# Kernel optimization log

Measured on AMD Instinct MI355X. Metric: run time of the kernel, lower is better.

Reference implementation:

```python
import jax, jax.numpy as jnp
import numpy as np
from jax import lax

H = 1024
L = 9


def setup_inputs() -> dict:
    key = jax.random.key(0)
    ks = jax.random.split(key, 10)
    B, T = 64, 512
    hidden_states = jax.random.normal(ks[0], (B, T, H), dtype=jnp.float32)
    attention_mask = jnp.ones((B, T), dtype=jnp.int32)
    labels = jax.random.randint(ks[1], (B, T), 0, L).astype(jnp.int64)
    W1 = 0.02 * jax.random.normal(ks[2], (H, H // 2), dtype=jnp.float32)
    b1 = jnp.zeros((H // 2,), dtype=jnp.float32)
    W2 = 0.02 * jax.random.normal(ks[3], (H // 2, L), dtype=jnp.float32)
    b2 = jnp.zeros((L,), dtype=jnp.float32)
    start_transitions = 0.1 * jax.random.normal(ks[4], (L,), dtype=jnp.float32)
    end_transitions = 0.1 * jax.random.normal(ks[5], (L,), dtype=jnp.float32)
    transitions = 0.1 * jax.random.normal(ks[6], (L, L), dtype=jnp.float32)
    return {"hidden_states": hidden_states, "attention_mask": attention_mask,
            "labels": labels, "W1": W1, "b1": b1, "W2": W2, "b2": b2,
            "start_transitions": start_transitions,
            "end_transitions": end_transitions, "transitions": transitions}


def crf_nll(logits, tags, mask, start_t, end_t, trans):
    """torchcrf negative mean log-likelihood. logits [B,T,L], tags [B,T], mask [B,T] bool."""
    emis = jnp.swapaxes(logits, 0, 1)          # [T,B,L]
    tg = jnp.swapaxes(tags, 0, 1)              # [T,B]
    m = jnp.swapaxes(mask, 0, 1).astype(logits.dtype)  # [T,B]

    # --- numerator: score of the gold path ---
    e0 = jnp.take_along_axis(emis[0], tg[0][:, None], axis=1)[:, 0]
    score0 = start_t[tg[0]] + e0

    def num_step(carry, inp):
        score, prev = carry
        e, t, mi = inp
        step = trans[prev, t] + jnp.take_along_axis(e, t[:, None], axis=1)[:, 0]
        score = score + step * mi
        prev = jnp.where(mi > 0, t, prev)
        return (score, prev), None

    (num, last_tag), _ = lax.scan(num_step, (score0, tg[0]), (emis[1:], tg[1:], m[1:]))
    num = num + end_t[last_tag]

    # --- denominator: forward algorithm (log partition) ---
    alpha0 = start_t[None, :] + emis[0]        # [B,L]

    def den_step(alpha, inp):
        e, mi = inp
        nxt = jax.nn.logsumexp(alpha[:, :, None] + trans[None, :, :] + e[:, None, :], axis=1)
        return jnp.where(mi[:, None] > 0, nxt, alpha), None

    alpha, _ = lax.scan(den_step, alpha0, (emis[1:], m[1:]))
    den = jax.nn.logsumexp(alpha + end_t[None, :], axis=1)

    return -jnp.mean(num - den)


def reference(hidden_states, attention_mask, labels, W1, b1, W2, b2,
              start_transitions, end_transitions, transitions):
    # dropout is identity in eval mode
    x = jax.nn.relu(hidden_states @ W1 + b1)
    logits = x @ W2 + b2                        # [B,T,L]

    valid = labels != -100
    crf_labels = jnp.where(valid, labels, 0)
    mask = (attention_mask.astype(bool)) & valid
    mask = mask.at[:, 0].set(True)              # first timestep always on

    loss = crf_nll(logits, crf_labels, mask,
                   start_transitions, end_transitions, transitions)
    return logits, loss
```

## Files before the change

### kernel.cpp

```cpp
#include <hip/hip_runtime.h>

#define T_  512
#define H_  1024
#define HC  512

typedef short short8 __attribute__((ext_vector_type(8)));
typedef float f32x16 __attribute__((ext_vector_type(16)));

__device__ __forceinline__ unsigned short f2bf(float x) {
  unsigned u = __float_as_uint(x);
  u += 0x7FFFu + ((u >> 16) & 1u);
  return (unsigned short)(u >> 16);
}
__device__ __forceinline__ float bf2f(unsigned short h) {
  return __uint_as_float(((unsigned)h) << 16);
}
__device__ __forceinline__ unsigned cvtpk(float lo, float hi) {
  unsigned r;
  asm("v_cvt_pk_bf16_f32 %0, %1, %2" : "=v"(r) : "v"(lo), "v"(hi));
  return r;
}
__device__ __forceinline__ void gload_lds16(const void* g, void* l) {
  __builtin_amdgcn_global_load_lds((const __attribute__((address_space(1))) unsigned*)g,
                                   (__attribute__((address_space(3))) unsigned*)l, 16, 0, 0);
}

__global__ void conv_w1(const float* __restrict__ w1, unsigned short* __restrict__ w1b) {
  int idx = blockIdx.x * 256 + threadIdx.x;
  int n = idx & 511, o = idx >> 9;
  const float* src = w1 + (size_t)(o * 8) * HC + n;
  float v[8];
  #pragma unroll
  for (int j = 0; j < 8; ++j) v[j] = src[j * HC];
  uint4 d;
  d.x = cvtpk(v[0], v[1]);
  d.y = cvtpk(v[2], v[3]);
  d.z = cvtpk(v[4], v[5]);
  d.w = cvtpk(v[6], v[7]);
  *(uint4*)(w1b + (size_t)idx * 8) = d;
}

__global__ __launch_bounds__(256, 2) void gemm1(
    const float* __restrict__ hs, const unsigned short* __restrict__ w1b,
    const float* __restrict__ b1, const float* __restrict__ w2,
    const float* __restrict__ b2, float* __restrict__ logits, float* __restrict__ wsE)
{
  __shared__ __align__(16) unsigned char smem[80128];
  const int tid  = threadIdx.x;
  const int lane = tid & 63;
  const int w    = tid >> 6;
  const int row0 = blockIdx.x * 64;

  f32x16 acc[2][4];
  #pragma unroll
  for (int m = 0; m < 2; ++m)
    #pragma unroll
    for (int n = 0; n < 4; ++n)
      #pragma unroll
      for (int e = 0; e < 16; ++e) acc[m][n][e] = 0.f;

  const int ar  = tid >> 2;
  const int akg = tid & 3;
  const float* aSrc = hs + (size_t)(row0 + ar) * H_ + akg * 8;
  const int aoff = ar * 64 + ((akg ^ ((ar >> 1) & 3)) * 16);

  {
    float4 av0 = *(const float4*)(aSrc);
    float4 av1 = *(const float4*)(aSrc + 4);
    unsigned char* bbase = smem + 4096;
    #pragma unroll
    for (int i = 0; i < 8; ++i) {
      int kg = i >> 1;
      int c0 = ((i & 1) * 4 + w) * 64;
      gload_lds16(w1b + ((size_t)kg * 512 + c0 + lane) * 8, bbase + (kg * 512 + c0) * 16);
    }
    uint4 ap;
    ap.x = cvtpk(av0.x, av0.y); ap.y = cvtpk(av0.z, av0.w);
    ap.z = cvtpk(av1.x, av1.y); ap.w = cvtpk(av1.z, av1.w);
    *(uint4*)(smem + aoff) = ap;
  }

  for (int kt = 0; kt < 31; ++kt) {
    const int cur = kt & 1, nxt = cur ^ 1;
    float4 av0 = *(const float4*)(aSrc + (kt + 1) * 32);
    float4 av1 = *(const float4*)(aSrc + (kt + 1) * 32 + 4);
    {
      unsigned char* bbase = smem + nxt * 36864 + 4096;
      int o0 = (kt + 1) * 4;
      #pragma unroll
      for (int i = 0; i < 8; ++i) {
        int kg = i >> 1;
        int c0 = ((i & 1) * 4 + w) * 64;
        gload_lds16(w1b + ((size_t)(o0 + kg) * 512 + c0 + lane) * 8,
                    bbase + (kg * 512 + c0) * 16);
      }
    }
    asm volatile("s_waitcnt vmcnt(10) lgkmcnt(0)" ::: "memory");
    __builtin_amdgcn_s_barrier();
    __builtin_amdgcn_sched_barrier(0);
    {
      const unsigned char* abase = smem + cur * 36864;
      const unsigned char* bbase = abase + 4096;
      #pragma unroll
      for (int ks = 0; ks < 2; ++ks) {
        const int kg = ks * 2 + (lane >> 5);
        short8 aF[2], bF[4];
        #pragma unroll
        for (int m = 0; m < 2; ++m) {
          int r = m * 32 + (lane & 31);
          aF[m] = *(const short8*)(abase + r * 64 + ((kg ^ ((r >> 1) & 3)) * 16));
        }
        #pragma unroll
        for (int n = 0; n < 4; ++n) {
          int c = w * 128 + n * 32 + (lane & 31);
          bF[n] = *(const short8*)(bbase + (kg * 512 + c) * 16);
        }
        #pragma unroll
        for (int m = 0; m < 2; ++m)
          #pragma unroll
          for (int n = 0; n < 4; ++n)
            acc[m][n] = __builtin_amdgcn_mfma_f32_32x32x16_bf16(aF[m], bF[n], acc[m][n], 0, 0, 0);
      }
    }
    {
      uint4 ap;
      ap.x = cvtpk(av0.x, av0.y); ap.y = cvtpk(av0.z, av0.w);
      ap.z = cvtpk(av1.x, av1.y); ap.w = cvtpk(av1.z, av1.w);
      *(uint4*)(smem + nxt * 36864 + aoff) = ap;
    }
  }
  asm volatile("s_waitcnt vmcnt(0) lgkmcnt(0)" ::: "memory");
  __builtin_amdgcn_s_barrier();
  __builtin_amdgcn_sched_barrier(0);
  {
    const unsigned char* abase = smem + 36864;
    const unsigned char* bbase = abase + 4096;
    #pragma unroll
    for (int ks = 0; ks < 2; ++ks) {
      const int kg = ks * 2 + (lane >> 5);
      short8 aF[2], bF[4];
      #pragma unroll
      for (int m = 0; m < 2; ++m) {
        int r = m * 32 + (lane & 31);
        aF[m] = *(const short8*)(abase + r * 64 + ((kg ^ ((r >> 1) & 3)) * 16));
      }
      #pragma unroll
      for (int n = 0; n < 4; ++n) {
        int c = w * 128 + n * 32 + (lane & 31);
        bF[n] = *(const short8*)(bbase + (kg * 512 + c) * 16);
      }
      #pragma unroll
      for (int m = 0; m < 2; ++m)
        #pragma unroll
        for (int n = 0; n < 4; ++n)
          acc[m][n] = __builtin_amdgcn_mfma_f32_32x32x16_bf16(aF[m], bF[n], acc[m][n], 0, 0, 0);
    }
  }
  __syncthreads();

  float b1v[4];
  #pragma unroll
  for (int n = 0; n < 4; ++n) b1v[n] = b1[w * 128 + n * 32 + (lane & 31)];

  #pragma unroll
  for (int m = 0; m < 2; ++m)
    #pragma unroll
    for (int n = 0; n < 4; ++n) {
      int col = w * 128 + n * 32 + (lane & 31);
      int csw = col & 7;
      unsigned char* cbase = smem + col * 128 + (lane >> 5) * 8;
      #pragma unroll
      for (int q = 0; q < 4; ++q) {
        float v0 = fmaxf(acc[m][n][q * 4 + 0] + b1v[n], 0.f);
        float v1 = fmaxf(acc[m][n][q * 4 + 1] + b1v[n], 0.f);
        float v2 = fmaxf(acc[m][n][q * 4 + 2] + b1v[n], 0.f);
        float v3 = fmaxf(acc[m][n][q * 4 + 3] + b1v[n], 0.f);
        uint2 d;
        d.x = cvtpk(v0, v1);
        d.y = cvtpk(v2, v3);
        *(uint2*)(cbase + (((4 * m + q) ^ csw) * 16)) = d;
      }
    }

  unsigned short* ldsW2 = (unsigned short*)(smem + 65536);
  float* sAcc = (float*)(smem + 77824);
  {
    int c0 = tid * 2;
    #pragma unroll
    for (int cc = c0; cc < c0 + 2; ++cc)
      #pragma unroll
      for (int l = 0; l < 9; ++l) ldsW2[cc * 12 + l] = f2bf(w2[cc * 9 + l]);
    for (int i = tid; i < 576; i += 256) sAcc[i] = 0.f;
  }
  __syncthreads();

  {
    int r = tid & 63, ch = tid >> 6;
    int rblk = r >> 3, rlow = r & 7;
    float s[9];
    #pragma unroll
    for (int l = 0; l < 9; ++l) s[l] = 0.f;
    for (int c = ch * 128; c < ch * 128 + 128; ++c) {
      float xv = bf2f(*(const unsigned short*)(smem + c * 128 + ((rblk ^ (c & 7)) * 16) + rlow * 2));
      uint2 wa = *(const uint2*)(ldsW2 + c * 12);
      uint2 wb = *(const uint2*)(ldsW2 + c * 12 + 4);
      unsigned wcv = *(const unsigned*)(ldsW2 + c * 12 + 8);
      s[0] = fmaf(xv, __uint_as_float(wa.x << 16), s[0]);
      s[1] = fmaf(xv, __uint_as_float(wa.x & 0xFFFF0000u), s[1]);
      s[2] = fmaf(xv, __uint_as_float(wa.y << 16), s[2]);
      s[3] = fmaf(xv, __uint_as_float(wa.y & 0xFFFF0000u), s[3]);
      s[4] = fmaf(xv, __uint_as_float(wb.x << 16), s[4]);
      s[5] = fmaf(xv, __uint_as_float(wb.x & 0xFFFF0000u), s[5]);
      s[6] = fmaf(xv, __uint_as_float(wb.y << 16), s[6]);
      s[7] = fmaf(xv, __uint_as_float(wb.y & 0xFFFF0000u), s[7]);
      s[8] = fmaf(xv, __uint_as_float(wcv << 16), s[8]);
    }
    #pragma unroll
    for (int l = 0; l < 9; ++l) atomicAdd(&sAcc[r * 9 + l], s[l]);
  }
  __syncthreads();

  {
    int bb = row0 >> 9, t0g = row0 & 511;
    for (int v = tid; v < 576; v += 256) {
      int r = v / 9, l = v - r * 9;
      float val = sAcc[v] + b2[l];
      logits[(size_t)(row0 + r) * 9 + l] = val;
      wsE[(size_t)((t0g + r) * 9 + l) * 64 + bb] = __expf(val);
    }
  }
}

#define NCH 64
#define CHL 8
__global__ __launch_bounds__(64, 1) void crf_chunks(
    const float* __restrict__ wsE, const int* __restrict__ labels,
    const int* __restrict__ amask, const float* __restrict__ logits,
    const float* __restrict__ trans, float* __restrict__ wsG)
{
  __shared__ float sT[81];
  int b = threadIdx.x;
  for (int i = b; i < 81; i += 64) sT[i] = trans[i];
  __syncthreads();
  int c = blockIdx.x;

  float eT[81];
  #pragma unroll
  for (int i = 0; i < 81; ++i) eT[i] = __expf(sT[i]);

  float G[81];
  #pragma unroll
  for (int i = 0; i < 9; ++i)
    #pragma unroll
    for (int j = 0; j < 9; ++j) G[i * 9 + j] = (i == j) ? 1.f : 0.f;

  float logC = 0.f, sumN = 0.f;
  int ft = -1, lt = -1, prevL = -1;

  int tstart = (c == 0) ? 1 : c * CHL;
  int tend = c * CHL + CHL;

  for (int t = tstart; t < tend; ++t) {
    int lab = labels[b * T_ + t];
    int am  = amask[b * T_ + t];
    bool valid = (lab != -100);
    int tag = valid ? lab : 0;
    bool m = (am != 0) && valid;

    float E[9];
    #pragma unroll
    for (int j = 0; j < 9; ++j) E[j] = wsE[(size_t)(t * 9 + j) * 64 + b];

    float emis = logits[(size_t)b * (T_ * 9) + t * 9 + tag];
    int pidx = (prevL < 0 ? 0 : prevL) * 9 + tag;
    float trTerm = (prevL >= 0) ? sT[pidx] : 0.f;
    sumN += m ? (emis + trTerm) : 0.f;
    ft = (m && ft < 0) ? tag : ft;
    lt = m ? tag : lt;
    prevL = m ? tag : prevL;

    #pragma unroll
    for (int i = 0; i < 9; ++i) {
      float nG[9];
      #pragma unroll
      for (int j = 0; j < 9; ++j) {
        float s = G[i * 9 + 0] * eT[j];
        #pragma unroll
        for (int k = 1; k < 9; ++k) s = fmaf(G[i * 9 + k], eT[k * 9 + j], s);
        nG[j] = s * E[j];
      }
      #pragma unroll
      for (int j = 0; j < 9; ++j) G[i * 9 + j] = m ? nG[j] : G[i * 9 + j];
    }
    float mx = G[0];
    #pragma unroll
    for (int e = 1; e < 81; ++e) mx = fmaxf(mx, G[e]);
    float rv = 1.0f / mx;
    logC += __logf(mx);
    #pragma unroll
    for (int e = 0; e < 81; ++e) G[e] *= rv;
  }

  float* o = wsG + (size_t)c * 88 * 64 + b;
  #pragma unroll
  for (int e = 0; e < 81; ++e) o[e * 64] = G[e];
  o[81 * 64] = logC;
  o[82 * 64] = sumN;
  o[83 * 64] = __int_as_float(ft);
  o[84 * 64] = __int_as_float(lt);
}

__global__ __launch_bounds__(64, 1) void crf_fold(
    const float* __restrict__ wsG, const float* __restrict__ trans,
    float* __restrict__ wsG2)
{
  __shared__ float sT[81];
  int b = threadIdx.x;
  for (int i = b; i < 81; i += 64) sT[i] = trans[i];
  __syncthreads();
  int f = blockIdx.x;

  float G[81];
  #pragma unroll
  for (int i = 0; i < 9; ++i)
    #pragma unroll
    for (int j = 0; j < 9; ++j) G[i * 9 + j] = (i == j) ? 1.f : 0.f;
  float logC = 0.f, sumN = 0.f;
  int ft = -1, lt = -1;

  for (int cc = 0; cc < 8; ++cc) {
    const float* g = wsG + (size_t)(f * 8 + cc) * 88 * 64 + b;
    float Gm[81];
    #pragma unroll
    for (int e = 0; e < 81; ++e) Gm[e] = g[e * 64];
    float lC = g[81 * 64], sN = g[82 * 64];
    int fte = __float_as_int(g[83 * 64]);
    int lte = __float_as_int(g[84 * 64]);

    #pragma unroll
    for (int i = 0; i < 9; ++i) {
      float row[9];
      #pragma unroll
      for (int j = 0; j < 9; ++j) {
        float s = G[i * 9 + 0] * Gm[j];
        #pragma unroll
        for (int k = 1; k < 9; ++k) s = fmaf(G[i * 9 + k], Gm[k * 9 + j], s);
        row[j] = s;
      }
      #pragma unroll
      for (int j = 0; j < 9; ++j) G[i * 9 + j] = row[j];
    }
    float mx = G[0];
    #pragma unroll
    for (int e = 1; e < 81; ++e) mx = fmaxf(mx, G[e]);
    logC += lC + __logf(mx);
    float rv = 1.0f / mx;
    #pragma unroll
    for (int e = 0; e < 81; ++e) G[e] *= rv;

    if (fte >= 0) {
      sumN += sN + (lt >= 0 ? sT[lt * 9 + fte] : 0.f);
      if (ft < 0) ft = fte;
      lt = lte;
    }
  }

  float* o = wsG2 + (size_t)f * 88 * 64 + b;
  #pragma unroll
  for (int e = 0; e < 81; ++e) o[e * 64] = G[e];
  o[81 * 64] = logC;
  o[82 * 64] = sumN;
  o[83 * 64] = __int_as_float(ft);
  o[84 * 64] = __int_as_float(lt);
}

__global__ __launch_bounds__(64, 1) void crf_final(
    const float* __restrict__ wsE, const int* __restrict__ labels,
    const float* __restrict__ logits,
    const float* __restrict__ start_t, const float* __restrict__ end_t,
    const float* __restrict__ trans, const float* __restrict__ wsG2,
    float* __restrict__ out_loss)
{
  __shared__ float sT[81];
  int b = threadIdx.x;
  for (int i = b; i < 81; i += 64) sT[i] = trans[i];
  __syncthreads();

  int lab0 = labels[b * T_];
  int tag0 = (lab0 != -100) ? lab0 : 0;
  float num = start_t[tag0] + logits[(size_t)b * (T_ * 9) + tag0];
  int prev = tag0;

  float P[9];
  #pragma unroll
  for (int j = 0; j < 9; ++j) P[j] = __expf(start_t[j]) * wsE[j * 64 + b];
  float mx = P[0];
  #pragma unroll
  for (int j = 1; j < 9; ++j) mx = fmaxf(mx, P[j]);
  float C = __logf(mx);
  float rv = 1.0f / mx;
  #pragma unroll
  for (int j = 0; j < 9; ++j) P[j] *= rv;

  for (int c = 0; c < 8; ++c) {
    const float* g = wsG2 + (size_t)c * 88 * 64 + b;
    float Gm[81];
    #pragma unroll
    for (int e = 0; e < 81; ++e) Gm[e] = g[e * 64];
    float logC = g[81 * 64];
    float sumN = g[82 * 64];
    int ft = __float_as_int(g[83 * 64]);
    int lt = __float_as_int(g[84 * 64]);

    float nP[9];
    #pragma unroll
    for (int j = 0; j < 9; ++j) {
      float s = P[0] * Gm[j];
      #pragma unroll
      for (int i = 1; i < 9; ++i) s = fmaf(P[i], Gm[i * 9 + j], s);
      nP[j] = s;
    }
    float mxs = nP[0];
    #pragma unroll
    for (int j = 1; j < 9; ++j) mxs = fmaxf(mxs, nP[j]);
    float rvs = 1.0f / mxs;
    C += logC + __logf(mxs);
    #pragma unroll
    for (int j = 0; j < 9; ++j) P[j] = nP[j] * rvs;

    if (ft >= 0) {
      num += sumN + sT[prev * 9 + ft];
      prev = lt;
    }
  }

  float sfin = 0.f;
  #pragma unroll
  for (int j = 0; j < 9; ++j) sfin = fmaf(P[j], __expf(end_t[j]), sfin);
  float den = C + __logf(sfin);
  num += end_t[prev];
  float d = num - den;
  #pragma unroll
  for (int off = 32; off > 0; off >>= 1) d += __shfl_down(d, off);
  if (b == 0) out_loss[0] = -d * (1.0f / 64.0f);
}

extern "C" void kernel_launch(void* const* d_in, const int* in_sizes, int n_in,
                              void* d_out, int out_size, void* d_ws, size_t ws_size,
                              hipStream_t stream) {
  (void)in_sizes; (void)n_in; (void)out_size; (void)ws_size;
  const float* hs     = (const float*)d_in[0];
  const int*   am     = (const int*)  d_in[1];
  const int*   labels = (const int*)  d_in[2];
  const float* w1     = (const float*)d_in[3];
  const float* b1     = (const float*)d_in[4];
  const float* w2     = (const float*)d_in[5];
  const float* b2     = (const float*)d_in[6];
  const float* st     = (const float*)d_in[7];
  const float* en     = (const float*)d_in[8];
  const float* tr     = (const float*)d_in[9];
  float* out = (float*)d_out;

  unsigned short* wsBn = (unsigned short*)d_ws;
  float*          wsE  = (float*)((char*)d_ws + 1048576);
  float*          wsG  = (float*)((char*)d_ws + 2228224);
  float*          wsG2 = (float*)((char*)d_ws + 3670016);

  conv_w1   <<<256, 256, 0, stream>>>(w1, wsBn);
  gemm1     <<<512, 256, 0, stream>>>(hs, wsBn, b1, w2, b2, out, wsE);
  crf_chunks<<<64,  64,  0, stream>>>(wsE, labels, am, out, tr, wsG);
  crf_fold  <<<8,   64,  0, stream>>>(wsG, tr, wsG2);
  crf_final <<<1,   64,  0, stream>>>(wsE, labels, out, st, en, tr, wsG2, out + 294912);
}
```

Before: 299.2 us.

## Double GEMM block to 512 threads and split CRF scan into more chunks

```diff
diff --git a/kernel.cpp b/kernel.cpp
--- a/kernel.cpp
+++ b/kernel.cpp
@@ -40,7 +40,7 @@
   *(uint4*)(w1b + (size_t)idx * 8) = d;
 }
 
-__global__ __launch_bounds__(256, 2) void gemm1(
+__global__ __launch_bounds__(512, 4) void gemm1(
     const float* __restrict__ hs, const unsigned short* __restrict__ w1b,
     const float* __restrict__ b1, const float* __restrict__ w2,
     const float* __restrict__ b2, float* __restrict__ logits, float* __restrict__ wsE)
@@ -51,122 +51,112 @@
   const int w    = tid >> 6;
   const int row0 = blockIdx.x * 64;
 
-  f32x16 acc[2][4];
+  f32x16 acc[2][2];
   #pragma unroll
   for (int m = 0; m < 2; ++m)
     #pragma unroll
-    for (int n = 0; n < 4; ++n)
+    for (int n = 0; n < 2; ++n)
       #pragma unroll
       for (int e = 0; e < 16; ++e) acc[m][n][e] = 0.f;
 
-  const int ar  = tid >> 2;
-  const int akg = tid & 3;
-  const float* aSrc = hs + (size_t)(row0 + ar) * H_ + akg * 8;
-  const int aoff = ar * 64 + ((akg ^ ((ar >> 1) & 3)) * 16);
+  const int ar   = tid >> 3;
+  const int aseg = tid & 7;
+  const float* aSrc = hs + (size_t)(row0 + ar) * H_ + aseg * 4;
+  const int aoff = (aseg >> 1) * 1024 + ar * 16 + (aseg & 1) * 8;
+
+  const int bkg = w >> 1;
+  const int bc1 = (w & 1) * 256;
 
   {
-    float4 av0 = *(const float4*)(aSrc);
-    float4 av1 = *(const float4*)(aSrc + 4);
-    unsigned char* bbase = smem + 4096;
-    #pragma unroll
-    for (int i = 0; i < 8; ++i) {
-      int kg = i >> 1;
-      int c0 = ((i & 1) * 4 + w) * 64;
-      gload_lds16(w1b + ((size_t)kg * 512 + c0 + lane) * 8, bbase + (kg * 512 + c0) * 16);
-    }
-    uint4 ap;
-    ap.x = cvtpk(av0.x, av0.y); ap.y = cvtpk(av0.z, av0.w);
-    ap.z = cvtpk(av1.x, av1.y); ap.w = cvtpk(av1.z, av1.w);
-    *(uint4*)(smem + aoff) = ap;
+    float4 av = *(const float4*)(aSrc);
+    #pragma unroll
+    for (int i = 0; i < 4; ++i) {
+      int c0 = bc1 + i * 64;
+      gload_lds16(w1b + ((size_t)bkg * 512 + c0 + lane) * 8,
+                  smem + 4096 + ((bkg * 512 + c0) * 16));
+    }
+    uint2 ap;
+    ap.x = cvtpk(av.x, av.y); ap.y = cvtpk(av.z, av.w);
+    *(uint2*)(smem + aoff) = ap;
   }
 
   for (int kt = 0; kt < 31; ++kt) {
     const int cur = kt & 1, nxt = cur ^ 1;
-    float4 av0 = *(const float4*)(aSrc + (kt + 1) * 32);
-    float4 av1 = *(const float4*)(aSrc + (kt + 1) * 32 + 4);
+    float4 av = *(const float4*)(aSrc + (kt + 1) * 32);
     {
-      unsigned char* bbase = smem + nxt * 36864 + 4096;
-      int o0 = (kt + 1) * 4;
-      #pragma unroll
-      for (int i = 0; i < 8; ++i) {
-        int kg = i >> 1;
-        int c0 = ((i & 1) * 4 + w) * 64;
-        gload_lds16(w1b + ((size_t)(o0 + kg) * 512 + c0 + lane) * 8,
-                    bbase + (kg * 512 + c0) * 16);
+      unsigned char* bb = smem + nxt * 36864 + 4096;
+      int O = (kt + 1) * 4 + bkg;
+      #pragma unroll
+      for (int i = 0; i < 4; ++i) {
+        int c0 = bc1 + i * 64;
+        gload_lds16(w1b + ((size_t)O * 512 + c0 + lane) * 8, bb + ((bkg * 512 + c0) * 16));
       }
     }
-    asm volatile("s_waitcnt vmcnt(10) lgkmcnt(0)" ::: "memory");
+    asm volatile("s_waitcnt vmcnt(5) lgkmcnt(0)" ::: "memory");
     __builtin_amdgcn_s_barrier();
     __builtin_amdgcn_sched_barrier(0);
     {
-      const unsigned char* abase = smem + cur * 36864;
-      const unsigned char* bbase = abase + 4096;
+      const unsigned char* ab = smem + cur * 36864;
+      const unsigned char* bb = ab + 4096;
       #pragma unroll
       for (int ks = 0; ks < 2; ++ks) {
         const int kg = ks * 2 + (lane >> 5);
-        short8 aF[2], bF[4];
-        #pragma unroll
-        for (int m = 0; m < 2; ++m) {
-          int r = m * 32 + (lane & 31);
-          aF[m] = *(const short8*)(abase + r * 64 + ((kg ^ ((r >> 1) & 3)) * 16));
-        }
-        #pragma unroll
-        for (int n = 0; n < 4; ++n) {
-          int c = w * 128 + n * 32 + (lane & 31);
-          bF[n] = *(const short8*)(bbase + (kg * 512 + c) * 16);
-        }
+        short8 aF[2], bF[2];
+        #pragma unroll
+        for (int m = 0; m < 2; ++m)
+          aF[m] = *(const short8*)(ab + kg * 1024 + (m * 32 + (lane & 31)) * 16);
+        #pragma unroll
+        for (int n = 0; n < 2; ++n)
+          bF[n] = *(const short8*)(bb + (kg * 512 + w * 64 + n * 32 + (lane & 31)) * 16);
+        __builtin_amdgcn_s_setprio(1);
         #pragma unroll
         for (int m = 0; m < 2; ++m)
           #pragma unroll
-          for (int n = 0; n < 4; ++n)
+          for (int n = 0; n < 2; ++n)
             acc[m][n] = __builtin_amdgcn_mfma_f32_32x32x16_bf16(aF[m], bF[n], acc[m][n], 0, 0, 0);
+        __builtin_amdgcn_s_setprio(0);
       }
     }
     {
-      uint4 ap;
-      ap.x = cvtpk(av0.x, av0.y); ap.y = cvtpk(av0.z, av0.w);
-      ap.z = cvtpk(av1.x, av1.y); ap.w = cvtpk(av1.z, av1.w);
-      *(uint4*)(smem + nxt * 36864 + aoff) = ap;
+      uint2 ap;
+      ap.x = cvtpk(av.x, av.y); ap.y = cvtpk(av.z, av.w);
+      *(uint2*)(smem + nxt * 36864 + aoff) = ap;
     }
   }
   asm volatile("s_waitcnt vmcnt(0) lgkmcnt(0)" ::: "memory");
   __builtin_amdgcn_s_barrier();
   __builtin_amdgcn_sched_barrier(0);
   {
-    const unsigned char* abase = smem + 36864;
-    const unsigned char* bbase = abase + 4096;
+    const unsigned char* ab = smem + 36864;
+    const unsigned char* bb = ab + 4096;
     #pragma unroll
     for (int ks = 0; ks < 2; ++ks) {
       const int kg = ks * 2 + (lane >> 5);
-      short8 aF[2], bF[4];
-      #pragma unroll
-      for (int m = 0; m < 2; ++m) {
-        int r = m * 32 + (lane & 31);
-        aF[m] = *(const short8*)(abase + r * 64 + ((kg ^ ((r >> 1) & 3)) * 16));
-      }
-      #pragma unroll
-      for (int n = 0; n < 4; ++n) {
-        int c = w * 128 + n * 32 + (lane & 31);
-        bF[n] = *(const short8*)(bbase + (kg * 512 + c) * 16);
-      }
+      short8 aF[2], bF[2];
       #pragma unroll
       for (int m = 0; m < 2; ++m)
-        #pragma unroll
-        for (int n = 0; n < 4; ++n)
+        aF[m] = *(const short8*)(ab + kg * 1024 + (m * 32 + (lane & 31)) * 16);
+      #pragma unroll
+      for (int n = 0; n < 2; ++n)
+        bF[n] = *(const short8*)(bb + (kg * 512 + w * 64 + n * 32 + (lane & 31)) * 16);
+      #pragma unroll
+      for (int m = 0; m < 2; ++m)
+        #pragma unroll
+        for (int n = 0; n < 2; ++n)
           acc[m][n] = __builtin_amdgcn_mfma_f32_32x32x16_bf16(aF[m], bF[n], acc[m][n], 0, 0, 0);
     }
   }
   __syncthreads();
 
-  float b1v[4];
-  #pragma unroll
-  for (int n = 0; n < 4; ++n) b1v[n] = b1[w * 128 + n * 32 + (lane & 31)];
+  float b1v[2];
+  #pragma unroll
+  for (int n = 0; n < 2; ++n) b1v[n] = b1[w * 64 + n * 32 + (lane & 31)];
 
   #pragma unroll
   for (int m = 0; m < 2; ++m)
     #pragma unroll
-    for (int n = 0; n < 4; ++n) {
-      int col = w * 128 + n * 32 + (lane & 31);
+    for (int n = 0; n < 2; ++n) {
+      int col = w * 64 + n * 32 + (lane & 31);
       int csw = col & 7;
       unsigned char* cbase = smem + col * 128 + (lane >> 5) * 8;
       #pragma unroll
@@ -185,12 +175,10 @@
   unsigned short* ldsW2 = (unsigned short*)(smem + 65536);
   float* sAcc = (float*)(smem + 77824);
   {
-    int c0 = tid * 2;
-    #pragma unroll
-    for (int cc = c0; cc < c0 + 2; ++cc)
-      #pragma unroll
-      for (int l = 0; l < 9; ++l) ldsW2[cc * 12 + l] = f2bf(w2[cc * 9 + l]);
-    for (int i = tid; i < 576; i += 256) sAcc[i] = 0.f;
+    int cc = tid;
+    #pragma unroll
+    for (int l = 0; l < 9; ++l) ldsW2[cc * 12 + l] = f2bf(w2[cc * 9 + l]);
+    for (int i = tid; i < 576; i += 512) sAcc[i] = 0.f;
   }
   __syncthreads();
 
@@ -200,7 +188,7 @@
     float s[9];
     #pragma unroll
     for (int l = 0; l < 9; ++l) s[l] = 0.f;
-    for (int c = ch * 128; c < ch * 128 + 128; ++c) {
+    for (int c = ch * 64; c < ch * 64 + 64; ++c) {
       float xv = bf2f(*(const unsigned short*)(smem + c * 128 + ((rblk ^ (c & 7)) * 16) + rlow * 2));
       uint2 wa = *(const uint2*)(ldsW2 + c * 12);
       uint2 wb = *(const uint2*)(ldsW2 + c * 12 + 4);
@@ -222,7 +210,7 @@
 
   {
     int bb = row0 >> 9, t0g = row0 & 511;
-    for (int v = tid; v < 576; v += 256) {
+    for (int v = tid; v < 576; v += 512) {
       int r = v / 9, l = v - r * 9;
       float val = sAcc[v] + b2[l];
       logits[(size_t)(row0 + r) * 9 + l] = val;
@@ -231,8 +219,8 @@
   }
 }
 
-#define NCH 64
-#define CHL 8
+#define NCH 128
+#define CHL 4
 __global__ __launch_bounds__(64, 1) void crf_chunks(
     const float* __restrict__ wsE, const int* __restrict__ labels,
     const int* __restrict__ amask, const float* __restrict__ logits,
@@ -402,7 +390,7 @@
   #pragma unroll
   for (int j = 0; j < 9; ++j) P[j] *= rv;
 
-  for (int c = 0; c < 8; ++c) {
+  for (int c = 0; c < 16; ++c) {
     const float* g = wsG2 + (size_t)c * 88 * 64 + b;
     float Gm[81];
     #pragma unroll
@@ -464,11 +452,11 @@
   unsigned short* wsBn = (unsigned short*)d_ws;
   float*          wsE  = (float*)((char*)d_ws + 1048576);
   float*          wsG  = (float*)((char*)d_ws + 2228224);
-  float*          wsG2 = (float*)((char*)d_ws + 3670016);
+  float*          wsG2 = (float*)((char*)d_ws + 5111808);
 
   conv_w1   <<<256, 256, 0, stream>>>(w1, wsBn);
-  gemm1     <<<512, 256, 0, stream>>>(hs, wsBn, b1, w2, b2, out, wsE);
-  crf_chunks<<<64,  64,  0, stream>>>(wsE, labels, am, out, tr, wsG);
-  crf_fold  <<<8,   64,  0, stream>>>(wsG, tr, wsG2);
+  gemm1     <<<512, 512, 0, stream>>>(hs, wsBn, b1, w2, b2, out, wsE);
+  crf_chunks<<<128, 64,  0, stream>>>(wsE, labels, am, out, tr, wsG);
+  crf_fold  <<<16,  64,  0, stream>>>(wsG, tr, wsG2);
   crf_final <<<1,   64,  0, stream>>>(wsE, labels, out, st, en, tr, wsG2, out + 294912);
 }
```

Result: no change. 299.4 us (+0.1%).
